# Kernel optimization log

Hardware: AMD Instinct MI355X
Metric: run time of the kernel (lower is better)

Reference implementation:

```python
import jax, jax.numpy as jnp
import numpy as np

# Tensor layout: x is [b, c, d, h, w, p, q, r] = [batch, channels, D, H, W, pd, ph, pw]
LETTERS = 'bcdhwpqr'

def axial_linear(x, W, b, axis, S, C):
    """LinearAlongDims1 over dims [1, axis]: jointly mixes channels and one
    spatial/patch axis. Torch flattens in (spatial, channel) order, so the
    (S*C, S*C) weight is reshaped to [S_out, C_out, S_in, C_in]."""
    a = LETTERS[axis]
    W4 = W.reshape(S, C, S, C)
    out_sub = LETTERS.replace('c', 'Y').replace(a, 'X')
    y = jnp.einsum(f'{LETTERS},XY{a}c->{out_sub}', x, W4)
    bshape = [1] * 8
    bshape[1] = C
    bshape[axis] = S
    return y + b.reshape(S, C).T.reshape(bshape)


def _make_linear_params(key, n):
    kw, kb = jax.random.split(key)
    bound = 1.0 / np.sqrt(n)
    W = jax.random.uniform(kw, (n, n), jnp.float32, -bound, bound)
    b = jax.random.uniform(kb, (n,), jnp.float32, -bound, bound)
    return W, b


def setup_inputs() -> dict:
    key = jax.random.key(0)
    ks = jax.random.split(key, 7)
    B, C, D, P = 2, 64, 16, 4
    x = jax.random.normal(ks[0], (B, C, D, D, D, P, P, P), jnp.float32)
    w_d, b_d = _make_linear_params(ks[1], C * D)      # image_d: dims [1,2]
    w_h, b_h = _make_linear_params(ks[2], C * D)      # image_h: dims [1,3]
    w_w, b_w = _make_linear_params(ks[3], C * D)      # image_w: dims [1,4]
    w_pd, b_pd = _make_linear_params(ks[4], C * P)    # patch_d: dims [1,5]
    w_ph, b_ph = _make_linear_params(ks[5], C * P)    # patch_h: dims [1,6]
    w_pw, b_pw = _make_linear_params(ks[6], C * P)    # patch_w: dims [1,7]
    return {
        'x': x,
        'w_d': w_d, 'b_d': b_d, 'w_h': w_h, 'b_h': b_h, 'w_w': w_w, 'b_w': b_w,
        'w_pd': w_pd, 'b_pd': b_pd, 'w_ph': w_ph, 'b_ph': b_ph,
        'w_pw': w_pw, 'b_pw': b_pw,
    }


def reference(x, w_d, b_d, w_h, b_h, w_w, b_w,
              w_pd, b_pd, w_ph, b_ph, w_pw, b_pw):
    C = x.shape[1]
    D = x.shape[2]
    P = x.shape[5]
    y = axial_linear(x, w_pd, b_pd, 5, P, C)
    y = y + axial_linear(x, w_ph, b_ph, 6, P, C)
    y = y + axial_linear(x, w_pw, b_pw, 7, P, C)
    y = y + axial_linear(x, w_d, b_d, 2, D, C)
    y = y + axial_linear(x, w_h, b_h, 3, D, C)
    y = y + axial_linear(x, w_w, b_w, 4, D, C)
    # shapes match -> leaky_relu + residual (module returns y; gn(x) is discarded)
    y = x + jax.nn.leaky_relu(y, negative_slope=0.01)
    return y
```

## Files before the change

### kernel.cpp

```cpp
#include <hip/hip_runtime.h>

typedef __attribute__((ext_vector_type(8))) short short8;
typedef __attribute__((ext_vector_type(4))) float floatx4;


__device__ __forceinline__ unsigned short f2bf(float f){
  unsigned int u = __float_as_uint(f);
  u += 0x7FFFu + ((u >> 16) & 1u);
  return (unsigned short)(u >> 16);
}

template<int AX>
__device__ __forceinline__ int tidx(int m, int a, int c){
  if      (AX==0){ int b=m>>14, t=m&16383;                         return (b<<24)|(c<<18)|(a<<14)|t; }
  else if (AX==1){ int b=m>>14, d=(m>>10)&15, t=m&1023;            return (b<<24)|(c<<18)|(d<<14)|(a<<10)|t; }
  else           { int b=m>>14, d=(m>>10)&15, h=(m>>6)&15, t=m&63; return (b<<24)|(c<<18)|(d<<14)|(h<<10)|(a<<6)|t; }
}

template<int AX>
__device__ __forceinline__ int srcbase(int m){
  if      (AX==0) return ((m>>14)<<24) | (((m>>10)&15)<<16) | (((m>>6)&15)<<12) | ((m&63)<<6);
  else if (AX==1) return ((m>>14)<<24) | (((m>>10)&15)<<20) | (((m>>6)&15)<<12) | ((m&63)<<6);
  else            return ((m>>14)<<24) | (((m>>10)&15)<<20) | (((m>>6)&15)<<16) | ((m&63)<<6);
}

#define ASYNC_CP16(g, l) \
  __builtin_amdgcn_global_load_lds( \
      (const __attribute__((address_space(1))) unsigned int*)(g), \
      (__attribute__((address_space(3))) unsigned int*)(l), 16, 0, 0)

__global__ __launch_bounds__(256) void castw_all(
    const float* __restrict__ wa, const float* __restrict__ wb, const float* __restrict__ wc,
    const float* __restrict__ wd_, const float* __restrict__ we, const float* __restrict__ wf,
    const float* __restrict__ bd_, const float* __restrict__ bh_, const float* __restrict__ bw_,
    const float* __restrict__ bpd_, const float* __restrict__ bph_, const float* __restrict__ bpw_,
    unsigned short* oa, unsigned short* ob, unsigned short* oc,
    unsigned short* od, unsigned short* oe, unsigned short* of_,
    float* __restrict__ Bimg, float* __restrict__ Bpat){
  int blk = blockIdx.x;
  if (blk < 6528){
    const float* src; unsigned short* dst; int idx;
    if (blk < 6144){ int wsel = blk >> 11, loc = blk & 2047;
      src = wsel==0?wa:(wsel==1?wb:wc); dst = wsel==0?oa:(wsel==1?ob:oc);
      idx = loc*256 + threadIdx.x; }
    else { int b2 = blk - 6144, wsel = b2 >> 7, loc = b2 & 127;
      src = wsel==0?wd_:(wsel==1?we:wf); dst = wsel==0?od:(wsel==1?oe:of_);
      idx = loc*256 + threadIdx.x; }
    float2 v = ((const float2*)src)[idx];
    ((unsigned int*)dst)[idx] = (unsigned int)f2bf(v.x) | ((unsigned int)f2bf(v.y) << 16);
  } else if (blk < 7552){
    int idx = (blk - 6528)*256 + threadIdx.x;
    int c = idx & 63, wv = (idx>>6)&15, hv = (idx>>10)&15, dv = idx>>14;
    Bimg[idx] = bd_[dv*64+c] + bh_[hv*64+c] + bw_[wv*64+c];
  } else {
    int idx = (blk - 7552)*256 + threadIdx.x;
    int c = idx & 63, tt = idx>>6;
    int p = tt>>4, q = (tt>>2)&3, r = tt&3;
    Bpat[idx] = bpd_[p*64+c] + bph_[q*64+c] + bpw_[r*64+c];
  }
}

__global__ __launch_bounds__(256) void transpose_cx(const float* __restrict__ x,
                                                    unsigned short* __restrict__ xt){
  __shared__ float T[64][65];
  int b  = blockIdx.x >> 12;
  int s0 = (blockIdx.x & 4095) * 64;
  int t = threadIdx.x;
  int cr = t >> 4, sq = t & 15;
  #pragma unroll
  for (int it = 0; it < 4; it++){
    int c = it*16 + cr;
    float4 v = *(const float4*)(x + (b<<24) + (c<<18) + s0 + sq*4);
    T[c][sq*4+0]=v.x; T[c][sq*4+1]=v.y; T[c][sq*4+2]=v.z; T[c][sq*4+3]=v.w;
  }
  __syncthreads();
  int sw = t >> 2, cq = t & 3;
  unsigned int pk[8];
  #pragma unroll
  for (int i=0;i<8;i++){
    float f0 = T[cq*16 + 2*i    ][sw];
    float f1 = T[cq*16 + 2*i + 1][sw];
    pk[i] = (unsigned int)f2bf(f0) | ((unsigned int)f2bf(f1) << 16);
  }
  uint4* dst = (uint4*)(xt + (b<<24) + ((s0 + sw)<<6) + cq*16);
  dst[0] = make_uint4(pk[0],pk[1],pk[2],pk[3]);
  dst[1] = make_uint4(pk[4],pk[5],pk[6],pk[7]);
}

template<int AXI, bool FIRST>
__device__ __forceinline__ void patch_axis(const unsigned short* Xs,
                                           const unsigned short* __restrict__ W,
                                           float* AccL, int w, int l16, int q8){
  floatx4 acc[4][2];
  #pragma unroll
  for (int nt=0;nt<4;nt++)
    #pragma unroll
    for (int mt=0;mt<2;mt++) acc[nt][mt] = (floatx4){0.f,0.f,0.f,0.f};

  #pragma unroll 2
  for (int kit = 0; kit < 8; kit++){
    int a = kit >> 1;
    short8 bf[2], af[4];
    int u = (AXI==0) ? (a*16 + l16)
          : (AXI==1) ? ((l16>>2)*16 + a*4 + (l16&3))
                     : ((l16>>2)*16 + (l16&3)*4 + a);
    int jg = ((kit & 1) << 2) + q8;
    #pragma unroll
    for (int mt = 0; mt < 2; mt++){
      int r = mt*64 + u;
      int j = jg ^ ((r ^ (r >> 3)) & 7);
      bf[mt] = *(const short8*)(Xs + r*64 + j*8);
    }
    #pragma unroll
    for (int nt = 0; nt < 4; nt++){
      int n = w*64 + nt*16 + l16;
      af[nt] = *(const short8*)(W + n*256 + kit*32 + q8*8);
    }
    #pragma unroll
    for (int nt=0; nt<4; nt++)
      #pragma unroll
      for (int mt=0; mt<2; mt++)
        acc[nt][mt] = __builtin_amdgcn_mfma_f32_16x16x32_bf16(af[nt], bf[mt], acc[nt][mt], 0,0,0);
  }

  int uo = (AXI==0) ? (w*16 + l16)
         : (AXI==1) ? ((l16>>2)*16 + w*4 + (l16&3))
                    : ((l16>>2)*16 + (l16&3)*4 + w);
  #pragma unroll
  for (int nt=0; nt<4; nt++)
    #pragma unroll
    for (int mt=0; mt<2; mt++){
      float* p = AccL + (mt*64 + uo)*65 + nt*16 + q8*4;
      #pragma unroll
      for (int rg=0; rg<4; rg++){
        if (FIRST) p[rg]  = acc[nt][mt][rg];
        else       p[rg] += acc[nt][mt][rg];
      }
    }
}

__global__ __launch_bounds__(256) void patch_fused(const unsigned short* __restrict__ xt,
    const unsigned short* __restrict__ Wp_, const unsigned short* __restrict__ Wq_,
    const unsigned short* __restrict__ Wr_, float* __restrict__ out){
  __shared__ float AccL[2*64*65];
  __shared__ unsigned short Xs[8192];
  int pp = blockIdx.x;
  int b = pp >> 11, dpair = pp & 2047;
  const unsigned short* xp = xt + (b<<24) + dpair*8192;
  int t = threadIdx.x, w = t>>6, lane = t&63, q8 = lane>>4, l16 = lane&15;

  #pragma unroll
  for (int i = 0; i < 4; i++){
    int L = i*256 + t;
    int r = L >> 3, jl = L & 7;
    int jg = jl ^ ((r ^ (r >> 3)) & 7);
    ASYNC_CP16(xp + r*64 + jg*8, Xs + i*2048 + w*512);
  }
  __syncthreads();

  patch_axis<0,true >(Xs, Wp_, AccL, w, l16, q8);
  __syncthreads();
  patch_axis<1,false>(Xs, Wq_, AccL, w, l16, q8);
  __syncthreads();
  patch_axis<2,false>(Xs, Wr_, AccL, w, l16, q8);
  __syncthreads();

  int sbase = dpair*128;
  #pragma unroll
  for (int it = 0; it < 32; it++){
    int lin = it*256 + t;
    int c = lin >> 7, rem = lin & 127, pt = rem >> 6, u = rem & 63;
    out[(b<<24) | (c<<18) | (sbase + pt*64 + u)] = AccL[(pt*64+u)*65 + c];
  }
}

template<int AX, int EPI>
__global__ __launch_bounds__(256) void gemm_img(const unsigned short* __restrict__ xt,
                                                const unsigned short* __restrict__ Wbf,
                                                float* __restrict__ out,
                                                const float* __restrict__ x,
                                                const float* __restrict__ Bimg,
                                                const float* __restrict__ Bpat){
  constexpr int K  = 1024;
  constexpr int SA = (AX==0)?(1<<20):(AX==1)?(1<<16):(1<<12);
  int mt = blockIdx.x >> 3;
  int nt = blockIdx.x & 7;

  __shared__ unsigned short Xs[128*32];
  __shared__ unsigned short Ws[128*32];

  int t = threadIdx.x, lane = t & 63, wid = t >> 6;
  int wn = (wid & 1) << 6, wm = (wid >> 1) << 6;
  int q = lane >> 4, l16 = lane & 15;

  floatx4 acc[4][4];
  #pragma unroll
  for (int i=0;i<4;i++)
    #pragma unroll
    for (int j=0;j<4;j++) acc[i][j] = (floatx4){0.f,0.f,0.f,0.f};

  const unsigned short* Wp = Wbf + (size_t)nt*128*K;

  int row = t >> 2;
  int jj  = (t & 3) ^ ((t >> 3) & 3);
  int base0 = srcbase<AX>(mt*128 + row);
  int base1 = srcbase<AX>(mt*128 + 64 + row);
  const unsigned short* wg0 = Wp + row*K + jj*8;
  const unsigned short* wg1 = Wp + (row+64)*K + jj*8;
  unsigned short* ldsX0 = Xs + wid*512;
  unsigned short* ldsX1 = Xs + 2048 + wid*512;
  unsigned short* ldsW0 = Ws + wid*512;
  unsigned short* ldsW1 = Ws + 2048 + wid*512;

  int xoff[4], woff[4];
  #pragma unroll
  for (int i=0;i<4;i++){
    int rx = wm + i*16 + l16; xoff[i] = rx*32 + ((q ^ ((rx>>1)&3))<<3);
    int rw = wn + i*16 + l16; woff[i] = rw*32 + ((q ^ ((rw>>1)&3))<<3);
  }

  for (int k0 = 0; k0 < K; k0 += 32){
    int aK = k0 >> 6;
    int cc = (k0 & 63) + jj*8;
    ASYNC_CP16(xt + base0 + aK*SA + cc, ldsX0);
    ASYNC_CP16(xt + base1 + aK*SA + cc, ldsX1);
    ASYNC_CP16(wg0 + k0, ldsW0);
    ASYNC_CP16(wg1 + k0, ldsW1);
    __syncthreads();

    short8 wf[4], xf[4];
    #pragma unroll
    for (int i=0;i<4;i++){
      wf[i] = *(const short8*)&Ws[woff[i]];
      xf[i] = *(const short8*)&Xs[xoff[i]];
    }
    #pragma unroll
    for (int i=0;i<4;i++)
      #pragma unroll
      for (int j=0;j<4;j++)
        acc[i][j] = __builtin_amdgcn_mfma_f32_16x16x32_bf16(wf[i], xf[j], acc[i][j], 0,0,0);
    __syncthreads();
  }

  #pragma unroll
  for (int i=0;i<4;i++){
    #pragma unroll
    for (int j=0;j<4;j++){
      int mg = mt*128 + wm + j*16 + l16;
      if (EPI){
        int d = (mg>>10)&15, h = (mg>>6)&15, tt = mg&63;
        int n0 = nt*128 + wn + i*16 + q*4;
        int a = n0 >> 6, c0 = n0 & 63;
        float4 bi = *(const float4*)(Bimg + (((d*16 + h)*16 + a)*64 + c0));
        float4 bp = *(const float4*)(Bpat + (tt*64 + c0));
        float bs0 = bi.x + bp.x, bs1 = bi.y + bp.y, bs2 = bi.z + bp.z, bs3 = bi.w + bp.w;
        #pragma unroll
        for (int rg=0; rg<4; rg++){
          int ng = n0 + rg;
          int idx = tidx<AX>(mg, ng>>6, ng&63);
          float bsum = (rg==0)?bs0:(rg==1)?bs1:(rg==2)?bs2:bs3;
          float y = out[idx] + acc[i][j][rg] + bsum;
          out[idx] = x[idx] + (y >= 0.f ? y : 0.01f*y);
        }
      } else {
        #pragma unroll
        for (int rg=0; rg<4; rg++){
          int ng = nt*128 + wn + i*16 + q*4 + rg;
          int idx = tidx<AX>(mg, ng>>6, ng&63);
          out[idx] += acc[i][j][rg];
        }
      }
    }
  }
}

extern "C" void kernel_launch(void* const* d_in, const int* in_sizes, int n_in,
                              void* d_out, int out_size, void* d_ws, size_t ws_size,
                              hipStream_t stream){
  const float* x = (const float*)d_in[0];
  const float* Wsrc[6] = {(const float*)d_in[1], (const float*)d_in[3], (const float*)d_in[5],
                          (const float*)d_in[7], (const float*)d_in[9], (const float*)d_in[11]};
  const float* Bsrc[6] = {(const float*)d_in[2], (const float*)d_in[4], (const float*)d_in[6],
                          (const float*)d_in[8], (const float*)d_in[10], (const float*)d_in[12]};
  float* out = (float*)d_out;
  char* ws = (char*)d_ws;

  const size_t welems[6] = {1024u*1024u, 1024u*1024u, 1024u*1024u,
                            256u*256u, 256u*256u, 256u*256u};
  size_t wOff[6], o = 0;
  for (int i=0;i<6;i++){ wOff[i] = o; o += welems[i]*2; }
  size_t xtOff = (o + 255) & ~(size_t)255;
  size_t bimgOff = xtOff + ((size_t)1u<<25)*2;
  size_t bpatOff = bimgOff + (size_t)16*16*16*64*4;
  unsigned short* xt = (unsigned short*)(ws + xtOff);
  float* Bimg = (float*)(ws + bimgOff);
  float* Bpat = (float*)(ws + bpatOff);
  unsigned short* Wbf[6];
  for (int i=0;i<6;i++) Wbf[i] = (unsigned short*)(ws + wOff[i]);

  castw_all<<<7616,256,0,stream>>>(Wsrc[0],Wsrc[1],Wsrc[2],Wsrc[3],Wsrc[4],Wsrc[5],
                                   Bsrc[0],Bsrc[1],Bsrc[2],Bsrc[3],Bsrc[4],Bsrc[5],
                                   Wbf[0],Wbf[1],Wbf[2],Wbf[3],Wbf[4],Wbf[5],
                                   Bimg, Bpat);
  transpose_cx<<<8192,256,0,stream>>>(x, xt);

  patch_fused<<<4096,256,0,stream>>>(xt, Wbf[3], Wbf[4], Wbf[5], out);

  gemm_img<0,0><<<2048,256,0,stream>>>(xt, Wbf[0], out, nullptr, nullptr, nullptr);
  gemm_img<1,0><<<2048,256,0,stream>>>(xt, Wbf[1], out, nullptr, nullptr, nullptr);
  gemm_img<2,1><<<2048,256,0,stream>>>(xt, Wbf[2], out, x, Bimg, Bpat);
}
```

Measured before the change: 881.7 us.

## Double-buffer LDS tiles in image GEMM and remap blocks across XCDs

The image-axis GEMM kernel now keeps two LDS buffers for the X and W tiles. The async copies for the next K-slice are issued before the MFMAs on the current slice, so global-to-LDS traffic can overlap compute, and each iteration needs one barrier instead of two. Block indices are also remapped so that the eight N-tiles of an M-tile run on the same XCD, which is meant to improve L2 reuse of the shared X rows. The cost is doubled LDS use per block, which may lower occupancy.

```diff
diff --git a/kernel.cpp b/kernel.cpp
--- a/kernel.cpp
+++ b/kernel.cpp
@@ -183,11 +183,13 @@
                                                 const float* __restrict__ Bpat){
   constexpr int K  = 1024;
   constexpr int SA = (AX==0)?(1<<20):(AX==1)?(1<<16):(1<<12);
-  int mt = blockIdx.x >> 3;
-  int nt = blockIdx.x & 7;
-
-  __shared__ unsigned short Xs[128*32];
-  __shared__ unsigned short Ws[128*32];
+  int B = blockIdx.x;
+  int xcd = B & 7, seq = B >> 3;
+  int nt = seq & 7;
+  int mt = (seq >> 3) * 8 + xcd;
+
+  __shared__ unsigned short Xs[2][4096];
+  __shared__ unsigned short Ws[2][4096];
 
   int t = threadIdx.x, lane = t & 63, wid = t >> 6;
   int wn = (wid & 1) << 6, wm = (wid >> 1) << 6;
@@ -207,10 +209,6 @@
   int base1 = srcbase<AX>(mt*128 + 64 + row);
   const unsigned short* wg0 = Wp + row*K + jj*8;
   const unsigned short* wg1 = Wp + (row+64)*K + jj*8;
-  unsigned short* ldsX0 = Xs + wid*512;
-  unsigned short* ldsX1 = Xs + 2048 + wid*512;
-  unsigned short* ldsW0 = Ws + wid*512;
-  unsigned short* ldsW1 = Ws + 2048 + wid*512;
 
   int xoff[4], woff[4];
   #pragma unroll
@@ -219,28 +217,37 @@
     int rw = wn + i*16 + l16; woff[i] = rw*32 + ((q ^ ((rw>>1)&3))<<3);
   }
 
+  #define STAGE_T(k0, s) do { \
+    int aK_ = (k0) >> 6; \
+    int cc_ = ((k0) & 63) + jj*8; \
+    ASYNC_CP16(xt + base0 + aK_*SA + cc_, &Xs[s][wid*512]); \
+    ASYNC_CP16(xt + base1 + aK_*SA + cc_, &Xs[s][2048 + wid*512]); \
+    ASYNC_CP16(wg0 + (k0), &Ws[s][wid*512]); \
+    ASYNC_CP16(wg1 + (k0), &Ws[s][2048 + wid*512]); \
+  } while(0)
+
+  STAGE_T(0, 0);
+  __syncthreads();
+
   for (int k0 = 0; k0 < K; k0 += 32){
-    int aK = k0 >> 6;
-    int cc = (k0 & 63) + jj*8;
-    ASYNC_CP16(xt + base0 + aK*SA + cc, ldsX0);
-    ASYNC_CP16(xt + base1 + aK*SA + cc, ldsX1);
-    ASYNC_CP16(wg0 + k0, ldsW0);
-    ASYNC_CP16(wg1 + k0, ldsW1);
-    __syncthreads();
+    int cur = (k0 >> 5) & 1;
+    if (k0 + 32 < K) STAGE_T(k0 + 32, cur ^ 1);
 
     short8 wf[4], xf[4];
     #pragma unroll
     for (int i=0;i<4;i++){
-      wf[i] = *(const short8*)&Ws[woff[i]];
-      xf[i] = *(const short8*)&Xs[xoff[i]];
+      wf[i] = *(const short8*)&Ws[cur][woff[i]];
+      xf[i] = *(const short8*)&Xs[cur][xoff[i]];
     }
     #pragma unroll
     for (int i=0;i<4;i++)
       #pragma unroll
       for (int j=0;j<4;j++)
         acc[i][j] = __builtin_amdgcn_mfma_f32_16x16x32_bf16(wf[i], xf[j], acc[i][j], 0,0,0);
+
     __syncthreads();
   }
+  #undef STAGE_T
 
   #pragma unroll
   for (int i=0;i<4;i++){
```

New measurement: 933.0 us. +5.8%, slower.
